# Kernel optimization log

Measured on AMD Instinct MI355X. Metric: run time of the kernel, lower is better.

Reference implementation:

```python
import jax, jax.numpy as jnp
import numpy as np

B, T, D, U = 64, 512, 512, 512


def setup_inputs() -> dict:
    key = jax.random.key(0)
    ks = jax.random.split(key, 5)
    inputs = jax.random.normal(ks[0], (B, T, D), dtype=jnp.float32)
    s = 1.0 / np.sqrt(U + D)
    Wf = jax.random.normal(ks[1], (U + D, U), dtype=jnp.float32) * s
    Wi = jax.random.normal(ks[2], (U + D, U), dtype=jnp.float32) * s
    Wc = jax.random.normal(ks[3], (U + D, U), dtype=jnp.float32) * s
    Wo = jax.random.normal(ks[4], (U + D, U), dtype=jnp.float32) * s
    bf = jnp.ones((U,), jnp.float32)   # forget gate bias initialized to ones
    bi = jnp.zeros((U,), jnp.float32)
    bc = jnp.zeros((U,), jnp.float32)
    bo = jnp.zeros((U,), jnp.float32)
    return {"inputs": inputs, "Wf": Wf, "bf": bf, "Wi": Wi, "bi": bi,
            "Wc": Wc, "bc": bc, "Wo": Wo, "bo": bo}


def reference(inputs, Wf, bf, Wi, bi, Wc, bc, Wo, bo):
    batch, length, _ = inputs.shape
    units = Wf.shape[1]
    h0 = jnp.zeros((batch, units), inputs.dtype)
    c0 = jnp.zeros((batch, units), inputs.dtype)

    def step(carry, x_t):
        h, c = carry
        z = jnp.concatenate([h, x_t], axis=1)  # [B, U+D]
        f = jax.nn.sigmoid(z @ Wf + bf)
        i = jax.nn.sigmoid(z @ Wi + bi)
        g = jnp.tanh(z @ Wc + bc)
        c_new = f * c + i * g
        o = jax.nn.sigmoid(z @ Wo + bo)
        h_new = o * jnp.tanh(c_new)
        return (h_new, c_new), h_new

    xs = jnp.transpose(inputs, (1, 0, 2))  # [T, B, D]
    _, hs = jax.lax.scan(step, (h0, c0), xs)
    return jnp.transpose(hs, (1, 0, 2))  # [B, T, U]
```

## Files before the change

### kernel.cpp

```cpp
#include <hip/hip_runtime.h>
#include <hip/hip_bf16.h>

typedef __attribute__((ext_vector_type(8))) short bf16x8;
typedef __attribute__((ext_vector_type(4))) float f32x4;

#define NB 64
#define NT 512
#define ND 512
#define NU 512

__device__ __forceinline__ unsigned short f2bf(float f) {
  union { float f; unsigned int u; } v; v.f = f;
  unsigned int r = v.u + 0x7fffu + ((v.u >> 16) & 1u);
  return (unsigned short)(r >> 16);
}
__device__ __forceinline__ float bf2f(unsigned short h) {
  union { unsigned int u; float f; } v; v.u = ((unsigned int)h) << 16;
  return v.f;
}
__device__ __forceinline__ float sigm(float x) {
  return 1.f / (1.f + __expf(-x));
}
__device__ __forceinline__ float tanh_f(float x) {
  float ax = fminf(fabsf(x), 15.f);
  float e = __expf(2.f * ax);
  float t = (e - 1.f) / (e + 1.f);
  return copysignf(t, x);
}


__global__ void k_cvt_x(const float* __restrict__ X, unsigned short* __restrict__ Xb, int n) {
  int i = (blockIdx.x * 256 + threadIdx.x) * 4;
  if (i < n) {
    float4 v = *(const float4*)(X + i);
    ushort4 o;
    o.x = f2bf(v.x); o.y = f2bf(v.y); o.z = f2bf(v.z); o.w = f2bf(v.w);
    *(ushort4*)(Xb + i) = o;
  }
}

__global__ void k_wx(const float* __restrict__ Wf, const float* __restrict__ Wi,
                     const float* __restrict__ Wc, const float* __restrict__ Wo,
                     unsigned short* __restrict__ Wt) {
  int idx = blockIdx.x * 256 + threadIdx.x;
  int c = idx >> 9, k = idx & 511;
  int gate = c & 3, u = c >> 2;
  const float* W = (gate == 0) ? Wf : (gate == 1) ? Wi : (gate == 2) ? Wc : Wo;
  Wt[idx] = f2bf(W[(512 + k) * 512 + u]);
}

__global__ void k_whpack(const float* __restrict__ Wf, const float* __restrict__ Wi,
                         const float* __restrict__ Wc, const float* __restrict__ Wo,
                         unsigned short* __restrict__ P) {
  int chunk = blockIdx.x * 256 + threadIdx.x;
  int lane = chunk & 63;
  int cgi = (chunk >> 6) & 1;
  int ks = (chunk >> 7) & 15;
  int j = chunk >> 11;
  int cl = cgi * 16 + (lane & 15);
  int u = j * 8 + (cl >> 2);
  int gate = cl & 3;
  const float* W = (gate == 0) ? Wf : (gate == 1) ? Wi : (gate == 2) ? Wc : Wo;
  int kb = ks * 32 + (lane >> 4) * 8;
  ushort4 lo, hi;
  lo.x = f2bf(W[(kb + 0) * 512 + u]); lo.y = f2bf(W[(kb + 1) * 512 + u]);
  lo.z = f2bf(W[(kb + 2) * 512 + u]); lo.w = f2bf(W[(kb + 3) * 512 + u]);
  hi.x = f2bf(W[(kb + 4) * 512 + u]); hi.y = f2bf(W[(kb + 5) * 512 + u]);
  hi.z = f2bf(W[(kb + 6) * 512 + u]); hi.w = f2bf(W[(kb + 7) * 512 + u]);
  *(ushort4*)(P + chunk * 8) = lo;
  *(ushort4*)(P + chunk * 8 + 4) = hi;
}


#define LDAP 72

__global__ void __launch_bounds__(256)
k_gemm_xproj(const unsigned short* __restrict__ Xb,
             const unsigned short* __restrict__ Wt,
             unsigned short* __restrict__ xproj) {
  __shared__ unsigned short As[128 * LDAP];
  __shared__ unsigned short Bs[128 * LDAP];
  const int tid = threadIdx.x;
  const int bid = blockIdx.x;
  const int mt = bid >> 4;
  const int ntile = bid & 15;
  const int m0 = mt * 128, n0 = ntile * 128;
  const int lane = tid & 63, w = tid >> 6;
  const int wm = w >> 1, wn = w & 1;

  const unsigned short* aSrc = Xb + (long)(m0 + (tid >> 3)) * 512 + (tid & 7) * 8;
  const unsigned short* bSrc = Wt + (long)(n0 + (tid >> 3)) * 512 + (tid & 7) * 8;
  const int ldsRow = (tid >> 3);
  const int ldsK = (tid & 7) * 8;

  f32x4 acc[4][4] = {};
  bf16x8 sa[4], sb[4];

#pragma unroll
  for (int c = 0; c < 4; c++) {
    sa[c] = *(const bf16x8*)(aSrc + (long)c * 32 * 512);
    sb[c] = *(const bf16x8*)(bSrc + (long)c * 32 * 512);
  }
  for (int kk = 0; kk < 8; kk++) {
    __syncthreads();
#pragma unroll
    for (int c = 0; c < 4; c++) {
      *(bf16x8*)(As + (c * 32 + ldsRow) * LDAP + ldsK) = sa[c];
      *(bf16x8*)(Bs + (c * 32 + ldsRow) * LDAP + ldsK) = sb[c];
    }
    __syncthreads();
    if (kk < 7) {
      const unsigned short* aS = aSrc + (kk + 1) * 64;
      const unsigned short* bS = bSrc + (kk + 1) * 64;
#pragma unroll
      for (int c = 0; c < 4; c++) {
        sa[c] = *(const bf16x8*)(aS + (long)c * 32 * 512);
        sb[c] = *(const bf16x8*)(bS + (long)c * 32 * 512);
      }
    }
#pragma unroll
    for (int ks = 0; ks < 2; ks++) {
      bf16x8 afr[4], bfr[4];
#pragma unroll
      for (int i = 0; i < 4; i++)
        afr[i] = *(const bf16x8*)(As + (wm * 64 + i * 16 + (lane & 15)) * LDAP + ks * 32 + (lane >> 4) * 8);
#pragma unroll
      for (int i = 0; i < 4; i++)
        bfr[i] = *(const bf16x8*)(Bs + (wn * 64 + i * 16 + (lane & 15)) * LDAP + ks * 32 + (lane >> 4) * 8);
#pragma unroll
      for (int i = 0; i < 4; i++)
#pragma unroll
        for (int jn = 0; jn < 4; jn++)
          acc[i][jn] = __builtin_amdgcn_mfma_f32_16x16x32_bf16(afr[i], bfr[jn], acc[i][jn], 0, 0, 0);
    }
  }
#pragma unroll
  for (int i = 0; i < 4; i++) {
    int row = m0 + wm * 64 + i * 16 + (lane >> 4) * 4;
#pragma unroll
    for (int jn = 0; jn < 4; jn++) {
      int col = n0 + wn * 64 + jn * 16 + (lane & 15);
#pragma unroll
      for (int r = 0; r < 4; r++)
        xproj[(long)(row + r) * 2048 + col] = f2bf(acc[i][jn][r]);
    }
  }
}


__device__ __forceinline__ float4 quad_transpose(f32x4 v, int g) {
  const bool odd = g & 1;
  float s0 = odd ? v[0] : v[1];
  float s1 = odd ? v[2] : v[3];
  float r0 = __shfl_xor(s0, 1, 64);
  float r1 = __shfl_xor(s1, 1, 64);
  float X0 = odd ? r0 : v[0];
  float X1 = odd ? v[1] : r0;
  float X2 = odd ? r1 : v[2];
  float X3 = odd ? v[3] : r1;
  const bool hi = g & 2;
  float t0 = hi ? X0 : X2;
  float t1 = hi ? X1 : X3;
  float q0 = __shfl_xor(t0, 2, 64);
  float q1 = __shfl_xor(t1, 2, 64);
  float4 y;
  y.x = hi ? q0 : X0;
  y.y = hi ? q1 : X1;
  y.z = hi ? X2 : q0;
  y.w = hi ? X3 : q1;
  return y;
}

__global__ void __launch_bounds__(256)
k_lstm(const unsigned short* __restrict__ xproj,
       const unsigned short* __restrict__ WhP,
       unsigned short* __restrict__ Hp,
       unsigned int* __restrict__ flags,
       const float* __restrict__ Bf, const float* __restrict__ Bi,
       const float* __restrict__ Bc, const float* __restrict__ Bo,
       float* __restrict__ out) {
  const int j = blockIdx.x;
  const int tid = threadIdx.x;
  const int lane = tid & 63;
  const int w = tid >> 6;

  bf16x8 bfrag[16][2];
#pragma unroll
  for (int ks = 0; ks < 16; ks++)
#pragma unroll
    for (int cgi = 0; cgi < 2; cgi++)
      bfrag[ks][cgi] = *(const bf16x8*)(WhP + ((((j * 16 + ks) * 2 + cgi) * 64 + lane) << 3));

  const int g = lane & 3;
  const int up = (lane & 15) >> 2;
  const int b = w * 16 + ((lane >> 4) << 2) + g;
  const int U0 = j * 8 + up;

  float c0 = 0.f, c1 = 0.f;
  const float bF0 = Bf[U0], bI0 = Bi[U0], bC0 = Bc[U0], bO0 = Bo[U0];
  const float bF1 = Bf[U0 + 4], bI1 = Bi[U0 + 4], bC1 = Bc[U0 + 4], bO1 = Bo[U0 + 4];

  const unsigned short* xp0 = xproj + (long)b * NT * 2048 + j * 32 + up * 4;
  float* out0 = out + (long)b * NT * NU + U0;

  const int chunk = ((j >> 2) * 4 + w) * 64 + (b & 15) + ((j & 3) << 4);
  unsigned short* hdst0 = Hp + (chunk << 3) + up;

  unsigned int* pubflag = flags + (j * 4 + w) * 16;
  const unsigned int* pollbase = flags + (lane * 4 + w) * 16;

  for (int t = 0; t < NT; t++) {
    ushort4 xa = *(const ushort4*)(xp0 + (long)t * 2048);
    ushort4 xb = *(const ushort4*)(xp0 + (long)t * 2048 + 16);

    if (t > 0) {
      while (!__all(__hip_atomic_load(pollbase, __ATOMIC_RELAXED,
                                      __HIP_MEMORY_SCOPE_AGENT) >= (unsigned)t)) {
      }
      __builtin_amdgcn_fence(__ATOMIC_ACQUIRE, "agent");
    }

    const unsigned short* hp = Hp + (t & 1) * 32768;
    bf16x8 af[16];
#pragma unroll
    for (int ks = 0; ks < 16; ks++)
      af[ks] = *(const bf16x8*)(hp + (((ks * 4 + w) * 64 + lane) << 3));

    f32x4 acc0 = {0.f, 0.f, 0.f, 0.f}, acc1 = {0.f, 0.f, 0.f, 0.f};
#pragma unroll
    for (int ks = 0; ks < 16; ks++) {
      acc0 = __builtin_amdgcn_mfma_f32_16x16x32_bf16(af[ks], bfrag[ks][0], acc0, 0, 0, 0);
      acc1 = __builtin_amdgcn_mfma_f32_16x16x32_bf16(af[ks], bfrag[ks][1], acc1, 0, 0, 0);
    }

    float4 G0 = quad_transpose(acc0, g);
    float4 G1 = quad_transpose(acc1, g);

    float f0 = sigm(G0.x + bf2f(xa.x) + bF0);
    float i0 = sigm(G0.y + bf2f(xa.y) + bI0);
    float g0 = tanh_f(G0.z + bf2f(xa.z) + bC0);
    float o0 = sigm(G0.w + bf2f(xa.w) + bO0);
    c0 = f0 * c0 + i0 * g0;
    float h0 = o0 * tanh_f(c0);
    float f1 = sigm(G1.x + bf2f(xb.x) + bF1);
    float i1 = sigm(G1.y + bf2f(xb.y) + bI1);
    float g1 = tanh_f(G1.z + bf2f(xb.z) + bC1);
    float o1 = sigm(G1.w + bf2f(xb.w) + bO1);
    c1 = f1 * c1 + i1 * g1;
    float h1 = o1 * tanh_f(c1);

    unsigned short* dst = hdst0 + ((t + 1) & 1) * 32768;
    __hip_atomic_store(dst, f2bf(h0), __ATOMIC_RELAXED, __HIP_MEMORY_SCOPE_AGENT);
    __hip_atomic_store(dst + 4, f2bf(h1), __ATOMIC_RELAXED, __HIP_MEMORY_SCOPE_AGENT);
    asm volatile("s_waitcnt vmcnt(0)" ::: "memory");
    if (lane == 0)
      __hip_atomic_store(pubflag, (unsigned)(t + 1), __ATOMIC_RELAXED,
                         __HIP_MEMORY_SCOPE_AGENT);

    out0[(long)t * NU] = h0;
    out0[(long)t * NU + 4] = h1;
  }
}


extern "C" void kernel_launch(void* const* d_in, const int* in_sizes, int n_in,
                              void* d_out, int out_size, void* d_ws, size_t ws_size,
                              hipStream_t stream) {
  const float* X  = (const float*)d_in[0];
  const float* Wf = (const float*)d_in[1];
  const float* Bf = (const float*)d_in[2];
  const float* Wi = (const float*)d_in[3];
  const float* Bi = (const float*)d_in[4];
  const float* Wc = (const float*)d_in[5];
  const float* Bc = (const float*)d_in[6];
  const float* Wo = (const float*)d_in[7];
  const float* Bo = (const float*)d_in[8];
  float* out = (float*)d_out;

  const size_t XB_OFF  = 0;
  const size_t HP_OFF  = 0;
  const size_t FL_OFF  = 131072;
  const size_t WT_OFF  = 33554432;
  const size_t XP_OFF  = 35651584;
  const size_t WHP_OFF = 169869312;
  const size_t NEEDED  = 171966464;
  if (ws_size < NEEDED) return;

  char* ws = (char*)d_ws;
  unsigned short* Xb    = (unsigned short*)(ws + XB_OFF);
  unsigned short* Wt    = (unsigned short*)(ws + WT_OFF);
  unsigned short* xproj = (unsigned short*)(ws + XP_OFF);
  unsigned short* WhP   = (unsigned short*)(ws + WHP_OFF);
  unsigned short* Hp    = (unsigned short*)(ws + HP_OFF);
  unsigned int*   flags = (unsigned int*)(ws + FL_OFF);

  k_cvt_x<<<16384, 256, 0, stream>>>(X, Xb, NB * NT * ND);
  k_wx<<<4096, 256, 0, stream>>>(Wf, Wi, Wc, Wo, Wt);
  k_whpack<<<512, 256, 0, stream>>>(Wf, Wi, Wc, Wo, WhP);
  k_gemm_xproj<<<4096, 256, 0, stream>>>(Xb, Wt, xproj);
  hipMemsetAsync(ws + HP_OFF, 0, 131072 + 16384, stream);

  const unsigned short* xp_a = xproj;
  const unsigned short* whp_a = WhP;
  unsigned short* hp_a = Hp;
  unsigned int* fl_a = flags;
  const float *bf_a = Bf, *bi_a = Bi, *bc_a = Bc, *bo_a = Bo;
  float* out_a = out;
  void* args[9] = {&xp_a, &whp_a, &hp_a, &fl_a, &bf_a, &bi_a, &bc_a, &bo_a, &out_a};
  hipLaunchCooperativeKernel((void*)k_lstm, dim3(64), dim3(256), args, 0, stream);
}
```

Baseline: 3.084 ms.

## Pack LSTM h handoff into dword stores and tighten inter-block flag polling

Remaps the recurrent-weight packing so each lane owns two adjacent units, which lets it publish both h values in one 32-bit atomic store, read gate inputs with one 16-byte load and write output with one nontemporal 8-byte store. Flags are packed contiguously instead of padded to 64 bytes each. The acquire fence is replaced by cache-coherent sc1 inline loads of h. The MFMA chain is split into two independent accumulators to shorten the dependency chain. This targets per-step latency of the serial recurrence, but it relies on sc1 loads for visibility, and packed flags may cause false sharing.

Result: slower. 3.304 ms (+7.1%).

```diff
diff --git a/kernel.cpp b/kernel.cpp
--- a/kernel.cpp
+++ b/kernel.cpp
@@ -3,6 +3,7 @@
 
 typedef __attribute__((ext_vector_type(8))) short bf16x8;
 typedef __attribute__((ext_vector_type(4))) float f32x4;
+typedef __attribute__((ext_vector_type(2))) float f32x2;
 
 #define NB 64
 #define NT 512
@@ -58,7 +59,7 @@
   int ks = (chunk >> 7) & 15;
   int j = chunk >> 11;
   int cl = cgi * 16 + (lane & 15);
-  int u = j * 8 + (cl >> 2);
+  int u = j * 8 + ((((cl & 15) >> 2)) << 1) + (cl >> 4);
   int gate = cl & 3;
   const float* W = (gate == 0) ? Wf : (gate == 1) ? Wi : (gate == 2) ? Wc : Wo;
   int kb = ks * 32 + (lane >> 4) * 8;
@@ -194,71 +195,81 @@
   const int g = lane & 3;
   const int up = (lane & 15) >> 2;
   const int b = w * 16 + ((lane >> 4) << 2) + g;
-  const int U0 = j * 8 + up;
+  const int U0 = j * 8 + 2 * up;
 
   float c0 = 0.f, c1 = 0.f;
   const float bF0 = Bf[U0], bI0 = Bi[U0], bC0 = Bc[U0], bO0 = Bo[U0];
-  const float bF1 = Bf[U0 + 4], bI1 = Bi[U0 + 4], bC1 = Bc[U0 + 4], bO1 = Bo[U0 + 4];
-
-  const unsigned short* xp0 = xproj + (long)b * NT * 2048 + j * 32 + up * 4;
+  const float bF1 = Bf[U0 + 1], bI1 = Bi[U0 + 1], bC1 = Bc[U0 + 1], bO1 = Bo[U0 + 1];
+
+  const unsigned short* xp0 = xproj + (long)b * NT * 2048 + j * 32 + up * 8;
   float* out0 = out + (long)b * NT * NU + U0;
 
   const int chunk = ((j >> 2) * 4 + w) * 64 + (b & 15) + ((j & 3) << 4);
-  unsigned short* hdst0 = Hp + (chunk << 3) + up;
-
-  unsigned int* pubflag = flags + (j * 4 + w) * 16;
-  const unsigned int* pollbase = flags + (lane * 4 + w) * 16;
+  unsigned int* hdst32 = (unsigned int*)Hp + (chunk << 2) + up;
+
+  unsigned int* pubflag = flags + w * 64 + j;
+  const unsigned int* pollbase = flags + w * 64 + lane;
 
   for (int t = 0; t < NT; t++) {
-    ushort4 xa = *(const ushort4*)(xp0 + (long)t * 2048);
-    ushort4 xb = *(const ushort4*)(xp0 + (long)t * 2048 + 16);
+    uint4 xv = *(const uint4*)(xp0 + (long)t * 2048);
 
     if (t > 0) {
       while (!__all(__hip_atomic_load(pollbase, __ATOMIC_RELAXED,
                                       __HIP_MEMORY_SCOPE_AGENT) >= (unsigned)t)) {
       }
-      __builtin_amdgcn_fence(__ATOMIC_ACQUIRE, "agent");
-    }
+    }
+    __builtin_amdgcn_sched_barrier(0);
 
     const unsigned short* hp = Hp + (t & 1) * 32768;
     bf16x8 af[16];
 #pragma unroll
-    for (int ks = 0; ks < 16; ks++)
-      af[ks] = *(const bf16x8*)(hp + (((ks * 4 + w) * 64 + lane) << 3));
-
-    f32x4 acc0 = {0.f, 0.f, 0.f, 0.f}, acc1 = {0.f, 0.f, 0.f, 0.f};
-#pragma unroll
     for (int ks = 0; ks < 16; ks++) {
-      acc0 = __builtin_amdgcn_mfma_f32_16x16x32_bf16(af[ks], bfrag[ks][0], acc0, 0, 0, 0);
-      acc1 = __builtin_amdgcn_mfma_f32_16x16x32_bf16(af[ks], bfrag[ks][1], acc1, 0, 0, 0);
-    }
+      asm volatile("global_load_dwordx4 %0, %1, off sc1"
+                   : "=v"(af[ks])
+                   : "v"(hp + (((ks * 4 + w) * 64 + lane) << 3)));
+    }
+    asm volatile("s_waitcnt vmcnt(0)" ::: "memory");
+    __builtin_amdgcn_sched_barrier(0);
+
+    f32x4 a0 = {0.f, 0.f, 0.f, 0.f}, a0b = {0.f, 0.f, 0.f, 0.f};
+    f32x4 a1 = {0.f, 0.f, 0.f, 0.f}, a1b = {0.f, 0.f, 0.f, 0.f};
+#pragma unroll
+    for (int ks = 0; ks < 8; ks++) {
+      a0 = __builtin_amdgcn_mfma_f32_16x16x32_bf16(af[ks], bfrag[ks][0], a0, 0, 0, 0);
+      a1 = __builtin_amdgcn_mfma_f32_16x16x32_bf16(af[ks], bfrag[ks][1], a1, 0, 0, 0);
+      a0b = __builtin_amdgcn_mfma_f32_16x16x32_bf16(af[ks + 8], bfrag[ks + 8][0], a0b, 0, 0, 0);
+      a1b = __builtin_amdgcn_mfma_f32_16x16x32_bf16(af[ks + 8], bfrag[ks + 8][1], a1b, 0, 0, 0);
+    }
+    f32x4 acc0 = a0 + a0b;
+    f32x4 acc1 = a1 + a1b;
 
     float4 G0 = quad_transpose(acc0, g);
     float4 G1 = quad_transpose(acc1, g);
 
-    float f0 = sigm(G0.x + bf2f(xa.x) + bF0);
-    float i0 = sigm(G0.y + bf2f(xa.y) + bI0);
-    float g0 = tanh_f(G0.z + bf2f(xa.z) + bC0);
-    float o0 = sigm(G0.w + bf2f(xa.w) + bO0);
+    float f0 = sigm(G0.x + bf2f((unsigned short)(xv.x & 0xffff)) + bF0);
+    float i0 = sigm(G0.y + bf2f((unsigned short)(xv.x >> 16)) + bI0);
+    float g0 = tanh_f(G0.z + bf2f((unsigned short)(xv.y & 0xffff)) + bC0);
+    float o0 = sigm(G0.w + bf2f((unsigned short)(xv.y >> 16)) + bO0);
     c0 = f0 * c0 + i0 * g0;
     float h0 = o0 * tanh_f(c0);
-    float f1 = sigm(G1.x + bf2f(xb.x) + bF1);
-    float i1 = sigm(G1.y + bf2f(xb.y) + bI1);
-    float g1 = tanh_f(G1.z + bf2f(xb.z) + bC1);
-    float o1 = sigm(G1.w + bf2f(xb.w) + bO1);
+    float f1 = sigm(G1.x + bf2f((unsigned short)(xv.z & 0xffff)) + bF1);
+    float i1 = sigm(G1.y + bf2f((unsigned short)(xv.z >> 16)) + bI1);
+    float g1 = tanh_f(G1.z + bf2f((unsigned short)(xv.w & 0xffff)) + bC1);
+    float o1 = sigm(G1.w + bf2f((unsigned short)(xv.w >> 16)) + bO1);
     c1 = f1 * c1 + i1 * g1;
     float h1 = o1 * tanh_f(c1);
 
-    unsigned short* dst = hdst0 + ((t + 1) & 1) * 32768;
-    __hip_atomic_store(dst, f2bf(h0), __ATOMIC_RELAXED, __HIP_MEMORY_SCOPE_AGENT);
-    __hip_atomic_store(dst + 4, f2bf(h1), __ATOMIC_RELAXED, __HIP_MEMORY_SCOPE_AGENT);
+    unsigned int hw = (unsigned int)f2bf(h0) | ((unsigned int)f2bf(h1) << 16);
+    __hip_atomic_store(hdst32 + (((t + 1) & 1) << 14), hw, __ATOMIC_RELAXED,
+                       __HIP_MEMORY_SCOPE_AGENT);
     asm volatile("s_waitcnt vmcnt(0)" ::: "memory");
     if (lane == 0)
       __hip_atomic_store(pubflag, (unsigned)(t + 1), __ATOMIC_RELAXED,
                          __HIP_MEMORY_SCOPE_AGENT);
-
-    out0[(long)t * NU] = h0;
-    out0[(long)t * NU + 4] = h1;
+    asm volatile("" ::: "memory");
+
+    f32x2 o2 = {h0, h1};
+    __builtin_nontemporal_store(o2, (f32x2*)(out0 + (long)t * NU));
   }
 }
 
@@ -298,7 +309,7 @@
   k_wx<<<4096, 256, 0, stream>>>(Wf, Wi, Wc, Wo, Wt);
   k_whpack<<<512, 256, 0, stream>>>(Wf, Wi, Wc, Wo, WhP);
   k_gemm_xproj<<<4096, 256, 0, stream>>>(Xb, Wt, xproj);
-  hipMemsetAsync(ws + HP_OFF, 0, 131072 + 16384, stream);
+  hipMemsetAsync(ws + HP_OFF, 0, 131072 + 1024, stream);
 
   const unsigned short* xp_a = xproj;
   const unsigned short* whp_a = WhP;
```
